# Performance work log

Hardware: AMD Instinct MI355X
Metric: run time of the kernel (lower is better)

The kernel has to match this reference:

```python
import jax, jax.numpy as jnp
import numpy as np

N_QUBITS = 8
N_LAYERS = 4
DIM = 2 ** N_QUBITS  # 256 state-vector

# PauliZ sign table: signs[i, idx] = +1 if bit of wire i in basis index idx is 0 else -1.
# Wire 0 is the most-significant axis (state axes ordered wire0..wire{n-1}).
_idx = np.arange(DIM)
SIGNS = np.stack([1.0 - 2.0 * ((_idx >> (N_QUBITS - 1 - i)) & 1) for i in range(N_QUBITS)]).astype(np.float32)  # [n, 256]


def _rx_mat(theta):
    c = jnp.cos(0.5 * theta).astype(jnp.complex64)
    s = (-1j * jnp.sin(0.5 * theta)).astype(jnp.complex64)
    return jnp.stack([jnp.stack([c, s]), jnp.stack([s, c])])  # [2,2]


def _rz_diag(theta):
    return jnp.stack([jnp.exp(-0.5j * theta), jnp.exp(0.5j * theta)]).astype(jnp.complex64)  # [2]


def _apply_1q(state, U, w):
    # state: (2,)*n complex64; apply 2x2 U on wire w
    st = jnp.moveaxis(state, w, 0).reshape(2, -1)
    st = U @ st
    return jnp.moveaxis(st.reshape((2,) * N_QUBITS), 0, w)


def _apply_diag(state, d, w):
    st = jnp.moveaxis(state, w, 0)
    st = st * d.reshape((2,) + (1,) * (N_QUBITS - 1))
    return jnp.moveaxis(st, 0, w)


def _cnot(state, c, t):
    st = jnp.moveaxis(state, (c, t), (0, 1))
    st = jnp.stack([st[0], st[1][::-1]], axis=0)  # flip target where control==1
    return jnp.moveaxis(st, (0, 1), (c, t))


def _circuit(angles, weights):
    # angles: [n_qubits], weights: [n_layers, 2, n_qubits] -> expvals [n_qubits]
    state = jnp.zeros((2,) * N_QUBITS, jnp.complex64).at[(0,) * N_QUBITS].set(1.0)
    for i in range(N_QUBITS):
        state = _apply_1q(state, _rx_mat(angles[i]), i)
        state = _apply_diag(state, _rz_diag(angles[i]), i)
    for l in range(N_LAYERS):
        for i in range(N_QUBITS):
            state = _apply_1q(state, _rx_mat(weights[l, 0, i]), i)
            state = _apply_diag(state, _rz_diag(weights[l, 1, i]), i)
        for i in range(N_QUBITS - 1):
            state = _cnot(state, i, i + 1)
    probs = jnp.abs(state.reshape(-1)) ** 2  # [256]
    return (probs @ SIGNS.T).astype(jnp.float32)  # [n_qubits] <Z_i>


def setup_inputs() -> dict:
    key = jax.random.key(0)
    B, D_IN, D_OUT = 8192, 1024, 1024
    ks = jax.random.split(key, 6)
    bound_in = np.sqrt(6.0 / D_IN)  # kaiming_uniform fan_in, linear
    bound_out = np.sqrt(6.0 / N_QUBITS)
    return {
        "x": jax.random.normal(ks[0], (B, D_IN), jnp.float32),
        "W_in": jax.random.uniform(ks[1], (N_QUBITS, D_IN), jnp.float32, -bound_in, bound_in),
        "b_in": jnp.zeros((N_QUBITS,), jnp.float32),
        "q_weights": jax.random.uniform(ks[2], (N_LAYERS, 2, N_QUBITS), jnp.float32, 0.0, 2.0 * np.pi),
        "W_out": jax.random.uniform(ks[3], (D_OUT, N_QUBITS), jnp.float32, -bound_out, bound_out),
        "b_out": jnp.zeros((D_OUT,), jnp.float32),
    }


def reference(x, W_in, b_in, q_weights, W_out, b_out):
    x_proj = x @ W_in.T + b_in                                   # [B, n_qubits]
    ev = jax.vmap(_circuit, in_axes=(0, None))(x_proj, q_weights)  # [B, n_qubits]
    return ev @ W_out.T + b_out                                   # [B, output_dim]
```

## Files before the change

### kernel.cpp

```cpp
#include <hip/hip_runtime.h>
#include <math.h>


__device__ __forceinline__ int f2i(float v) { return __float_as_int(v); }
__device__ __forceinline__ float i2f(int v) { return __int_as_float(v); }

template <int CTRL>
__device__ __forceinline__ float dppf(float v) {
    return i2f(__builtin_amdgcn_update_dpp(0, f2i(v), CTRL, 0xF, 0xF, true));
}

template <int ML>
__device__ __forceinline__ float gshm(float v) {
    static_assert(ML > 0 && ML < 64, "lane mask");
    if constexpr (ML == 1)      return dppf<0xB1>(v);
    else if constexpr (ML == 2) return dppf<0x4E>(v);
    else if constexpr (ML == 3) return dppf<0x1B>(v);
    else if constexpr (ML == 8) return dppf<0x128>(v);
    else if constexpr (ML < 32) return i2f(__builtin_amdgcn_ds_swizzle(f2i(v), 0x1F | (ML << 10)));
    else                        return __shfl_xor(v, ML, 64);
}

template <int L>
__device__ __forceinline__ float rdlane(float v) {
    return i2f(__builtin_amdgcn_readlane(f2i(v), L));
}

template <int ML, int MR, int ZL, int ZR>
__device__ __forceinline__ void ggate(float re[4], float im[4],
                                      float c1, float s1, float c2, float s2,
                                      int lane) {
    if constexpr (MR == 0) {
#pragma unroll
        for (int r = 0; r < 4; ++r) {
            float pre = gshm<ML>(re[r]);
            float pim = gshm<ML>(im[r]);
            re[r] = c1 * re[r] + s1 * pim;
            im[r] = c1 * im[r] - s1 * pre;
        }
    } else {
        float nre[4], nim[4];
#pragma unroll
        for (int r = 0; r < 4; ++r) {
            float pre, pim;
            if constexpr (ML != 0) {
                pre = gshm<ML>(re[r ^ MR]);
                pim = gshm<ML>(im[r ^ MR]);
            } else {
                pre = re[r ^ MR];
                pim = im[r ^ MR];
            }
            nre[r] = c1 * re[r] + s1 * pim;
            nim[r] = c1 * im[r] - s1 * pre;
        }
#pragma unroll
        for (int r = 0; r < 4; ++r) { re[r] = nre[r]; im[r] = nim[r]; }
    }
    float ssb;
    if constexpr (ZL == 0) ssb = -s2;
    else                   ssb = (__popc(lane & ZL) & 1) ? s2 : -s2;
#pragma unroll
    for (int r = 0; r < 4; ++r) {
        float ss = (__builtin_popcount(r & ZR) & 1) ? -ssb : ssb;
        float nr = c2 * re[r] - ss * im[r];
        im[r] = c2 * im[r] + ss * re[r];
        re[r] = nr;
    }
}

__global__ void __launch_bounds__(256, 4) qasa_kernel(
    const float* __restrict__ x, const float* __restrict__ W_in,
    const float* __restrict__ b_in, const float* __restrict__ qw,
    const float* __restrict__ W_out, const float* __restrict__ b_out,
    float* __restrict__ out)
{
    const int tid = threadIdx.x;
    const int lane = tid & 63;
    const size_t row = (size_t)blockIdx.x * 4 + (tid >> 6);

    float vc, vs;
    __sincosf(0.5f * qw[lane], &vs, &vc);

    float acc[8] = {0.f, 0.f, 0.f, 0.f, 0.f, 0.f, 0.f, 0.f};
    {
        const float4* xr = (const float4*)(x + row * 1024);
        const float4* w4 = (const float4*)W_in;
#pragma unroll
        for (int k = 0; k < 4; ++k) {
            float4 xv = xr[lane + 64 * k];
#pragma unroll
            for (int q = 0; q < 8; ++q) {
                float4 wv = w4[q * 256 + lane + 64 * k];
                acc[q] += xv.x * wv.x + xv.y * wv.y + xv.z * wv.z + xv.w * wv.w;
            }
        }
    }
#pragma unroll
    for (int q = 0; q < 8; ++q) {
        acc[q] += dppf<0xB1>(acc[q]);
        acc[q] += dppf<0x4E>(acc[q]);
        acc[q] += dppf<0x128>(acc[q]);
    }
    const int b0 = lane & 1, b1 = (lane >> 1) & 1, b3 = (lane >> 3) & 1;
    float t01 = b0 ? acc[1] : acc[0];
    float t23 = b0 ? acc[3] : acc[2];
    float t45 = b0 ? acc[5] : acc[4];
    float t67 = b0 ? acc[7] : acc[6];
    float ta = b1 ? t23 : t01;
    float tb = b1 ? t67 : t45;
    float A = b3 ? tb : ta;
    A += gshm<4>(A); A += gshm<16>(A); A += gshm<32>(A);
    A += b_in[b0 | (b1 << 1) | (b3 << 2)];
    float ec, es;
    __sincosf(0.5f * A, &es, &ec);

    float cc = ec * ec;
    float sq = es * es;
    float ncs = -(ec * es);

    float re[4], im[4];
    float P_re, P_im;
    {
        float Ar = rdlane<0>(cc), Br = rdlane<0>(sq);
        P_re = ((lane >> 5) & 1) ? Br : Ar;
        P_im = rdlane<0>(ncs);
    }
#define PMUL(W_) { \
        constexpr int L_ = ((W_) & 3) | ((((W_) >> 2) & 1) << 3); \
        float Ar = rdlane<L_>(cc), Br = rdlane<L_>(sq), Ai = rdlane<L_>(ncs); \
        float Fr = ((lane >> (5 - (W_))) & 1) ? Br : Ar; \
        float tr = P_re * Fr - P_im * Ai; \
        P_im = P_re * Ai + P_im * Fr; \
        P_re = tr; }
    PMUL(1) PMUL(2) PMUL(3) PMUL(4) PMUL(5)
#undef PMUL
    {
        float A6r = rdlane<10>(cc), B6r = rdlane<10>(sq), A6i = rdlane<10>(ncs);
        float A7r = rdlane<11>(cc), B7r = rdlane<11>(sq), A7i = rdlane<11>(ncs);
#pragma unroll
        for (int r = 0; r < 4; ++r) {
            float g6r = (r & 2) ? B6r : A6r;
            float g7r = (r & 1) ? B7r : A7r;
            float fre = g6r * g7r - A6i * A7i;
            float fim = g6r * A7i + A6i * g7r;
            re[r] = P_re * fre - P_im * fim;
            im[r] = P_re * fim + P_im * fre;
        }
    }

#define GG(Lx, W_, ML_, MR_, ZL_, ZR_) \
    ggate<ML_, MR_, ZL_, ZR_>(re, im, \
        rdlane<16 * (Lx) + (W_)>(vc), rdlane<16 * (Lx) + (W_)>(vs), \
        rdlane<16 * (Lx) + 8 + (W_)>(vc), rdlane<16 * (Lx) + 8 + (W_)>(vs), lane);

    GG(0,0, 32,0, 32,0)  GG(0,1, 16,0, 16,0)  GG(0,2, 8,0, 8,0)   GG(0,3, 4,0, 4,0)
    GG(0,4, 2,0, 2,0)    GG(0,5, 1,0, 1,0)    GG(0,6, 0,2, 0,2)   GG(0,7, 0,1, 0,1)
    GG(1,0, 48,0, 32,0)  GG(1,1, 24,0, 48,0)  GG(1,2, 12,0, 56,0) GG(1,3, 6,0, 60,0)
    GG(1,4, 3,0, 62,0)   GG(1,5, 1,2, 63,0)   GG(1,6, 0,3, 63,2)  GG(1,7, 0,1, 63,3)
    GG(2,0, 40,0, 32,0)  GG(2,1, 20,0, 16,0)  GG(2,2, 10,0, 40,0) GG(2,3, 5,0, 20,0)
    GG(2,4, 2,2, 42,0)   GG(2,5, 1,1, 21,0)   GG(2,6, 0,2, 42,2)  GG(2,7, 0,1, 21,1)
    GG(3,0, 60,0, 32,0)  GG(3,1, 30,0, 48,0)  GG(3,2, 15,0, 24,0) GG(3,3, 7,2, 12,0)
    GG(3,4, 3,3, 38,0)   GG(3,5, 1,3, 51,0)   GG(3,6, 0,3, 25,2)  GG(3,7, 0,1, 12,3)
#undef GG

    float p0 = re[0] * re[0] + im[0] * im[0];
    float p1 = re[1] * re[1] + im[1] * im[1];
    float p2 = re[2] * re[2] + im[2] * im[2];
    float p3 = re[3] * re[3] + im[3] * im[3];
    float q0 = (p0 + p1) + (p2 + p3);
    float q2 = (p0 + p1) - (p2 + p3);
    float q1 = (p0 + p2) - (p1 + p3);

    float v = q0;
    { float u = dppf<0xB1>(v);  v = (lane & 1)  ? (u - v) : (v + u); }
    { float u = dppf<0x4E>(v);  v = (lane & 2)  ? (u - v) : (v + u); }
    { float u = dppf<0x128>(v); v = (lane & 8)  ? (u - v) : (v + u); }
    { float u = gshm<4>(v);     v = (lane & 4)  ? (u - v) : (v + u); }
    { float u = gshm<16>(v);    v = (lane & 16) ? (u - v) : (v + u); }
    { float u = gshm<32>(v);    v = (lane & 32) ? (u - v) : (v + u); }
    const float EV0 = rdlane<32>(v), EV1 = rdlane<16>(v), EV2 = rdlane<8>(v);
    const float EV3 = rdlane<4>(v),  EV4 = rdlane<34>(v), EV5 = rdlane<17>(v);

    q2 += dppf<0xB1>(q2);
    q2 += dppf<0x4E>(q2);
    { float u = dppf<0x128>(q2); q2 = (lane & 8) ? (u - q2) : (q2 + u); }
    q2 += gshm<4>(q2); q2 += gshm<16>(q2); q2 += gshm<32>(q2);
    const float EV6 = rdlane<8>(q2);

    q1 += dppf<0xB1>(q1);
    q1 += dppf<0x4E>(q1);
    q1 += dppf<0x128>(q1);
    { float u = gshm<4>(q1); q1 = (lane & 4) ? (u - q1) : (q1 + u); }
    q1 += gshm<16>(q1); q1 += gshm<32>(q1);
    const float EV7 = rdlane<4>(q1);

    const float4* wo = (const float4*)W_out;
    const float4* bo = (const float4*)b_out;
    float4* orow = (float4*)(out + row * 1024);
#pragma unroll
    for (int jj = 0; jj < 4; ++jj) {
        const int c4 = lane + 64 * jj;
        float4 bias = bo[c4];
        float res[4];
#pragma unroll
        for (int c = 0; c < 4; ++c) {
            float4 wa = wo[2 * (4 * c4 + c)];
            float4 wb = wo[2 * (4 * c4 + c) + 1];
            res[c] = wa.x * EV0 + wa.y * EV1 + wa.z * EV2 + wa.w * EV3
                   + wb.x * EV4 + wb.y * EV5 + wb.z * EV6 + wb.w * EV7;
        }
        float4 o;
        o.x = bias.x + res[0]; o.y = bias.y + res[1];
        o.z = bias.z + res[2]; o.w = bias.w + res[3];
        orow[c4] = o;
    }
}

extern "C" void kernel_launch(void* const* d_in, const int* in_sizes, int n_in,
                              void* d_out, int out_size, void* d_ws, size_t ws_size,
                              hipStream_t stream) {
    const float* x     = (const float*)d_in[0];
    const float* W_in  = (const float*)d_in[1];
    const float* b_in  = (const float*)d_in[2];
    const float* qw    = (const float*)d_in[3];
    const float* W_out = (const float*)d_in[4];
    const float* b_out = (const float*)d_in[5];
    float* outp = (float*)d_out;

    const int B = in_sizes[0] / 1024;
    const int grid = B / 4;
    qasa_kernel<<<grid, 256, 0, stream>>>(x, W_in, b_in, qw, W_out, b_out, outp);
}
```

Baseline: 125.7 us.

## Fold layer-0 gates into product-state init and use packed f32x2 gate math

```diff
diff --git a/kernel.cpp b/kernel.cpp
--- a/kernel.cpp
+++ b/kernel.cpp
@@ -1,6 +1,8 @@
 #include <hip/hip_runtime.h>
 #include <math.h>
 
+
+typedef float f32x2 __attribute__((ext_vector_type(2)));
 
 __device__ __forceinline__ int f2i(float v) { return __float_as_int(v); }
 __device__ __forceinline__ float i2f(int v) { return __int_as_float(v); }
@@ -27,45 +29,39 @@
 }
 
 template <int ML, int MR, int ZL, int ZR>
-__device__ __forceinline__ void ggate(float re[4], float im[4],
+__device__ __forceinline__ void ggate(f32x2& reA, f32x2& reB, f32x2& imA, f32x2& imB,
                                       float c1, float s1, float c2, float s2,
                                       int lane) {
-    if constexpr (MR == 0) {
-#pragma unroll
-        for (int r = 0; r < 4; ++r) {
-            float pre = gshm<ML>(re[r]);
-            float pim = gshm<ML>(im[r]);
-            re[r] = c1 * re[r] + s1 * pim;
-            im[r] = c1 * im[r] - s1 * pre;
-        }
-    } else {
-        float nre[4], nim[4];
-#pragma unroll
-        for (int r = 0; r < 4; ++r) {
-            float pre, pim;
-            if constexpr (ML != 0) {
-                pre = gshm<ML>(re[r ^ MR]);
-                pim = gshm<ML>(im[r ^ MR]);
-            } else {
-                pre = re[r ^ MR];
-                pim = im[r ^ MR];
-            }
-            nre[r] = c1 * re[r] + s1 * pim;
-            nim[r] = c1 * im[r] - s1 * pre;
-        }
-#pragma unroll
-        for (int r = 0; r < 4; ++r) { re[r] = nre[r]; im[r] = nim[r]; }
-    }
-    float ssb;
-    if constexpr (ZL == 0) ssb = -s2;
-    else                   ssb = (__popc(lane & ZL) & 1) ? s2 : -s2;
-#pragma unroll
-    for (int r = 0; r < 4; ++r) {
-        float ss = (__builtin_popcount(r & ZR) & 1) ? -ssb : ssb;
-        float nr = c2 * re[r] - ss * im[r];
-        im[r] = c2 * im[r] + ss * re[r];
-        re[r] = nr;
-    }
+    f32x2 sReA, sReB, sImA, sImB;
+    if constexpr (MR == 0)      { sReA = reA;    sReB = reB;    sImA = imA;    sImB = imB; }
+    else if constexpr (MR == 1) { sReA = reA.yx; sReB = reB.yx; sImA = imA.yx; sImB = imB.yx; }
+    else if constexpr (MR == 2) { sReA = reB;    sReB = reA;    sImA = imB;    sImB = imA; }
+    else                        { sReA = reB.yx; sReB = reA.yx; sImA = imB.yx; sImB = imA.yx; }
+    f32x2 pReA, pReB, pImA, pImB;
+    if constexpr (ML != 0) {
+        pReA.x = gshm<ML>(sReA.x); pReA.y = gshm<ML>(sReA.y);
+        pReB.x = gshm<ML>(sReB.x); pReB.y = gshm<ML>(sReB.y);
+        pImA.x = gshm<ML>(sImA.x); pImA.y = gshm<ML>(sImA.y);
+        pImB.x = gshm<ML>(sImB.x); pImB.y = gshm<ML>(sImB.y);
+    } else { pReA = sReA; pReB = sReB; pImA = sImA; pImB = sImB; }
+    f32x2 nReA = c1 * reA + s1 * pImA;
+    f32x2 nReB = c1 * reB + s1 * pImB;
+    f32x2 nImA = c1 * imA - s1 * pReA;
+    f32x2 nImB = c1 * imB - s1 * pReB;
+    float base;
+    if constexpr (ZL == 0) base = -s2;
+    else                   base = (__popc(lane & ZL) & 1) ? s2 : -s2;
+    constexpr bool N1 = (ZR & 1) != 0;
+    constexpr bool N2 = ((ZR >> 1) & 1) != 0;
+    constexpr bool N3 = (((ZR & 1) ^ ((ZR >> 1) & 1)) != 0);
+    f32x2 ssA = { base, N1 ? -base : base };
+    f32x2 ssB = { N2 ? -base : base, N3 ? -base : base };
+    f32x2 tA = c2 * nReA - ssA * nImA;
+    f32x2 tB = c2 * nReB - ssB * nImB;
+    imA = c2 * nImA + ssA * nReA;
+    imB = c2 * nImB + ssB * nReB;
+    reA = tA;
+    reB = tB;
 }
 
 __global__ void __launch_bounds__(256, 4) qasa_kernel(
@@ -111,50 +107,64 @@
     float A = b3 ? tb : ta;
     A += gshm<4>(A); A += gshm<16>(A); A += gshm<32>(A);
     A += b_in[b0 | (b1 << 1) | (b3 << 2)];
-    float ec, es;
-    __sincosf(0.5f * A, &es, &ec);
-
-    float cc = ec * ec;
-    float sq = es * es;
-    float ncs = -(ec * es);
-
-    float re[4], im[4];
-    float P_re, P_im;
+    float ca, sa;
+    __sincosf(0.5f * A, &sa, &ca);
+
+    float ur = ca * ca, ui = -ca * sa, vr = sa * sa, vi = ui;
+    const int q = b0 | (b1 << 1) | (b3 << 2);
+    const int a1 = 4 * q, a2 = 4 * (q + 8);
+    float cx = i2f(__builtin_amdgcn_ds_bpermute(a1, f2i(vc)));
+    float sx = i2f(__builtin_amdgcn_ds_bpermute(a1, f2i(vs)));
+    float cz = i2f(__builtin_amdgcn_ds_bpermute(a2, f2i(vc)));
+    float sz = i2f(__builtin_amdgcn_ds_bpermute(a2, f2i(vs)));
+    float ur1 = cx * ur + sx * vi, ui1 = cx * ui - sx * vr;
+    float vr1 = cx * vr + sx * ui, vi1 = cx * vi - sx * ur;
+    float ur2 = cz * ur1 + sz * ui1, ui2 = cz * ui1 - sz * ur1;
+    float vr2 = cz * vr1 - sz * vi1, vi2 = cz * vi1 + sz * vr1;
+
+    float Pr, Pi;
     {
-        float Ar = rdlane<0>(cc), Br = rdlane<0>(sq);
-        P_re = ((lane >> 5) & 1) ? Br : Ar;
-        P_im = rdlane<0>(ncs);
-    }
-#define PMUL(W_) { \
-        constexpr int L_ = ((W_) & 3) | ((((W_) >> 2) & 1) << 3); \
-        float Ar = rdlane<L_>(cc), Br = rdlane<L_>(sq), Ai = rdlane<L_>(ncs); \
-        float Fr = ((lane >> (5 - (W_))) & 1) ? Br : Ar; \
-        float tr = P_re * Fr - P_im * Ai; \
-        P_im = P_re * Ai + P_im * Fr; \
-        P_re = tr; }
-    PMUL(1) PMUL(2) PMUL(3) PMUL(4) PMUL(5)
+        float fur = rdlane<0>(ur2), fui = rdlane<0>(ui2);
+        float fvr = rdlane<0>(vr2), fvi = rdlane<0>(vi2);
+        bool b = (lane >> 5) & 1;
+        Pr = b ? fvr : fur;
+        Pi = b ? fvi : fui;
+    }
+#define PMUL(W_, L_) { \
+        float fur = rdlane<L_>(ur2), fui = rdlane<L_>(ui2); \
+        float fvr = rdlane<L_>(vr2), fvi = rdlane<L_>(vi2); \
+        bool b = (lane >> (5 - (W_))) & 1; \
+        float fr = b ? fvr : fur, fi = b ? fvi : fui; \
+        float tr = Pr * fr - Pi * fi; \
+        Pi = Pr * fi + Pi * fr; \
+        Pr = tr; }
+    PMUL(1, 1) PMUL(2, 2) PMUL(3, 3) PMUL(4, 8) PMUL(5, 9)
 #undef PMUL
+    f32x2 reA, reB, imA, imB;
     {
-        float A6r = rdlane<10>(cc), B6r = rdlane<10>(sq), A6i = rdlane<10>(ncs);
-        float A7r = rdlane<11>(cc), B7r = rdlane<11>(sq), A7i = rdlane<11>(ncs);
+        float u6r = rdlane<10>(ur2), u6i = rdlane<10>(ui2);
+        float v6r = rdlane<10>(vr2), v6i = rdlane<10>(vi2);
+        float u7r = rdlane<11>(ur2), u7i = rdlane<11>(ui2);
+        float v7r = rdlane<11>(vr2), v7i = rdlane<11>(vi2);
+        float rr[4], ii[4];
 #pragma unroll
         for (int r = 0; r < 4; ++r) {
-            float g6r = (r & 2) ? B6r : A6r;
-            float g7r = (r & 1) ? B7r : A7r;
-            float fre = g6r * g7r - A6i * A7i;
-            float fim = g6r * A7i + A6i * g7r;
-            re[r] = P_re * fre - P_im * fim;
-            im[r] = P_re * fim + P_im * fre;
+            float g6r_ = (r & 2) ? v6r : u6r, g6i_ = (r & 2) ? v6i : u6i;
+            float g7r_ = (r & 1) ? v7r : u7r, g7i_ = (r & 1) ? v7i : u7i;
+            float fr = g6r_ * g7r_ - g6i_ * g7i_;
+            float fi = g6r_ * g7i_ + g6i_ * g7r_;
+            rr[r] = Pr * fr - Pi * fi;
+            ii[r] = Pr * fi + Pi * fr;
         }
+        reA = (f32x2){ rr[0], rr[1] };  reB = (f32x2){ rr[2], rr[3] };
+        imA = (f32x2){ ii[0], ii[1] };  imB = (f32x2){ ii[2], ii[3] };
     }
 
 #define GG(Lx, W_, ML_, MR_, ZL_, ZR_) \
-    ggate<ML_, MR_, ZL_, ZR_>(re, im, \
+    ggate<ML_, MR_, ZL_, ZR_>(reA, reB, imA, imB, \
         rdlane<16 * (Lx) + (W_)>(vc), rdlane<16 * (Lx) + (W_)>(vs), \
         rdlane<16 * (Lx) + 8 + (W_)>(vc), rdlane<16 * (Lx) + 8 + (W_)>(vs), lane);
 
-    GG(0,0, 32,0, 32,0)  GG(0,1, 16,0, 16,0)  GG(0,2, 8,0, 8,0)   GG(0,3, 4,0, 4,0)
-    GG(0,4, 2,0, 2,0)    GG(0,5, 1,0, 1,0)    GG(0,6, 0,2, 0,2)   GG(0,7, 0,1, 0,1)
     GG(1,0, 48,0, 32,0)  GG(1,1, 24,0, 48,0)  GG(1,2, 12,0, 56,0) GG(1,3, 6,0, 60,0)
     GG(1,4, 3,0, 62,0)   GG(1,5, 1,2, 63,0)   GG(1,6, 0,3, 63,2)  GG(1,7, 0,1, 63,3)
     GG(2,0, 40,0, 32,0)  GG(2,1, 20,0, 16,0)  GG(2,2, 10,0, 40,0) GG(2,3, 5,0, 20,0)
@@ -163,10 +173,10 @@
     GG(3,4, 3,3, 38,0)   GG(3,5, 1,3, 51,0)   GG(3,6, 0,3, 25,2)  GG(3,7, 0,1, 12,3)
 #undef GG
 
-    float p0 = re[0] * re[0] + im[0] * im[0];
-    float p1 = re[1] * re[1] + im[1] * im[1];
-    float p2 = re[2] * re[2] + im[2] * im[2];
-    float p3 = re[3] * re[3] + im[3] * im[3];
+    float p0 = reA.x * reA.x + imA.x * imA.x;
+    float p1 = reA.y * reA.y + imA.y * imA.y;
+    float p2 = reB.x * reB.x + imB.x * imB.x;
+    float p3 = reB.y * reB.y + imB.y * imB.y;
     float q0 = (p0 + p1) + (p2 + p3);
     float q2 = (p0 + p1) - (p2 + p3);
     float q1 = (p0 + p2) - (p1 + p3);
@@ -194,6 +204,8 @@
     q1 += gshm<16>(q1); q1 += gshm<32>(q1);
     const float EV7 = rdlane<4>(q1);
 
+    const f32x2 E01 = { EV0, EV1 }, E23 = { EV2, EV3 };
+    const f32x2 E45 = { EV4, EV5 }, E67 = { EV6, EV7 };
     const float4* wo = (const float4*)W_out;
     const float4* bo = (const float4*)b_out;
     float4* orow = (float4*)(out + row * 1024);
@@ -206,8 +218,9 @@
         for (int c = 0; c < 4; ++c) {
             float4 wa = wo[2 * (4 * c4 + c)];
             float4 wb = wo[2 * (4 * c4 + c) + 1];
-            res[c] = wa.x * EV0 + wa.y * EV1 + wa.z * EV2 + wa.w * EV3
-                   + wb.x * EV4 + wb.y * EV5 + wb.z * EV6 + wb.w * EV7;
+            f32x2 acc2 = E01 * (f32x2){ wa.x, wa.y } + E23 * (f32x2){ wa.z, wa.w }
+                       + E45 * (f32x2){ wb.x, wb.y } + E67 * (f32x2){ wb.z, wb.w };
+            res[c] = acc2.x + acc2.y;
         }
         float4 o;
         o.x = bias.x + res[0]; o.y = bias.y + res[1];
```

Measured after the change: 124.9 us. About the same (-0.7%).
